# Performance work log

Hardware: AMD Instinct MI355X
Metric: run time of the kernel (lower is better)

The kernel has to match this reference:

```python
import jax, jax.numpy as jnp
import numpy as np

N = 32768; D = 384; P = 3; CORR_D = 2 * 49 * P * P  # 882
G_KK = 4096; G_JK = 512
EPS = 1e-3  # LayerNorm eps in the torch module

FLOAT_NAMES = ("net","inp","corr","corr_w1","corr_b1","corr_w2","corr_b2","corr_ln_g","corr_ln_b","corr_w3","corr_b3","norm_g","norm_b","c1_w1","c1_b1","c1_w2","c1_b2","c2_w1","c2_b1","c2_w2","c2_b2","kk_fw","kk_fb","kk_gw","kk_gb","kk_hw","kk_hb","ij_fw","ij_fb","ij_gw","ij_gb","ij_hw","ij_hb","g_ln1_g","g_ln1_b","g1_gw","g1_gb","g1_r1w","g1_r1b","g1_r2w","g1_r2b","g_ln2_g","g_ln2_b","g2_gw","g2_gb","g2_r1w","g2_r1b","g2_r2w","g2_r2b","d_w","d_b","w_w","w_b")

def _ln(x, g, b):
    m = jnp.mean(x, -1, keepdims=True)
    v = jnp.mean((x - m) ** 2, -1, keepdims=True)
    return (x - m) * jax.lax.rsqrt(v + EPS) * g + b

def _mlp2(x, w1, b1, w2, b2):
    return jax.nn.relu(x @ w1 + b1) @ w2 + b2

def _gated_residual(x, gw, gb, r1w, r1b, r2w, r2b):
    gate = jax.nn.sigmoid(x @ gw + gb)
    res = jax.nn.relu(x @ r1w + r1b) @ r2w + r2b
    return x + gate * res

def _soft_agg(x, jx, fw, fb, gw, gb, hw, hb, num_groups):
    # x: [N, D]; jx: [N] group ids -> group-wise softmax weighted sum
    logits = x @ gw + gb
    feats = x @ fw + fb
    gmax = jax.ops.segment_max(logits, jx, num_segments=num_groups)
    e = jnp.exp(logits - gmax[jx])
    den = jax.ops.segment_sum(e, jx, num_segments=num_groups)
    w = e / (den[jx] + 1e-12)
    y = jax.ops.segment_sum(feats * w, jx, num_segments=num_groups)
    return (y @ hw + hb)[jx]

def _forward(p, nix, njx, ukk, ujk):
    # corr encoder MLP
    h = jax.nn.relu(p["corr"] @ p["corr_w1"] + p["corr_b1"]) @ p["corr_w2"] + p["corr_b2"]
    h = jax.nn.relu(_ln(h, p["corr_ln_g"], p["corr_ln_b"])) @ p["corr_w3"] + p["corr_b3"]
    net = p["net"] + p["inp"] + h
    net = _ln(net, p["norm_g"], p["norm_b"])
    mask_ix = (nix >= 0).astype(net.dtype).reshape(1, -1, 1)
    mask_jx = (njx >= 0).astype(net.dtype).reshape(1, -1, 1)
    net = net + _mlp2(mask_ix * net[:, nix], p["c1_w1"], p["c1_b1"], p["c1_w2"], p["c1_b2"])
    net = net + _mlp2(mask_jx * net[:, njx], p["c2_w1"], p["c2_b1"], p["c2_w2"], p["c2_b2"])
    net = net + _soft_agg(net[0], ukk, p["kk_fw"], p["kk_fb"], p["kk_gw"], p["kk_gb"], p["kk_hw"], p["kk_hb"], G_KK)[None]
    net = net + _soft_agg(net[0], ujk, p["ij_fw"], p["ij_fb"], p["ij_gw"], p["ij_gb"], p["ij_hw"], p["ij_hb"], G_JK)[None]
    net = _ln(net, p["g_ln1_g"], p["g_ln1_b"])
    net = _gated_residual(net, p["g1_gw"], p["g1_gb"], p["g1_r1w"], p["g1_r1b"], p["g1_r2w"], p["g1_r2b"])
    net = _ln(net, p["g_ln2_g"], p["g_ln2_b"])
    net = _gated_residual(net, p["g2_gw"], p["g2_gb"], p["g2_r1w"], p["g2_r1b"], p["g2_r2w"], p["g2_r2b"])
    r = jax.nn.relu(net)
    d = r @ p["d_w"] + p["d_b"]               # GradClip is identity in forward
    w = jax.nn.sigmoid(r @ p["w_w"] + p["w_b"])
    return net, d, w

def setup_inputs() -> dict:
    key = jax.random.key(0)
    it = iter(jax.random.split(key, 64))
    def pr(*shape):
        return jax.random.normal(next(it), shape, dtype=jnp.float32) * 0.02
    z = lambda *s: jnp.zeros(s, jnp.float32)
    o = lambda *s: jnp.ones(s, jnp.float32)
    inp = {
        "net": jax.random.normal(next(it), (1, N, D), dtype=jnp.float32),
        "inp": jax.random.normal(next(it), (1, N, D), dtype=jnp.float32),
        "corr": jax.random.normal(next(it), (1, N, CORR_D), dtype=jnp.float32),
        "nix": jax.random.randint(next(it), (N,), 0, N),
        "njx": jax.random.randint(next(it), (N,), 0, N),
        "ukk": jax.random.randint(next(it), (N,), 0, G_KK),
        "ujk": jax.random.randint(next(it), (N,), 0, G_JK),
        "corr_w1": pr(CORR_D, D), "corr_b1": z(D), "corr_w2": pr(D, D), "corr_b2": z(D),
        "corr_ln_g": o(D), "corr_ln_b": z(D), "corr_w3": pr(D, D), "corr_b3": z(D),
        "norm_g": o(D), "norm_b": z(D),
        "c1_w1": pr(D, D), "c1_b1": z(D), "c1_w2": pr(D, D), "c1_b2": z(D),
        "c2_w1": pr(D, D), "c2_b1": z(D), "c2_w2": pr(D, D), "c2_b2": z(D),
        "kk_fw": pr(D, D), "kk_fb": z(D), "kk_gw": pr(D, D), "kk_gb": z(D), "kk_hw": pr(D, D), "kk_hb": z(D),
        "ij_fw": pr(D, D), "ij_fb": z(D), "ij_gw": pr(D, D), "ij_gb": z(D), "ij_hw": pr(D, D), "ij_hb": z(D),
        "g_ln1_g": o(D), "g_ln1_b": z(D),
        "g1_gw": pr(D, D), "g1_gb": z(D), "g1_r1w": pr(D, D), "g1_r1b": z(D), "g1_r2w": pr(D, D), "g1_r2b": z(D),
        "g_ln2_g": o(D), "g_ln2_b": z(D),
        "g2_gw": pr(D, D), "g2_gb": z(D), "g2_r1w": pr(D, D), "g2_r1b": z(D), "g2_r2w": pr(D, D), "g2_r2b": z(D),
        "d_w": pr(D, 2), "d_b": z(2), "w_w": pr(D, 2), "w_b": z(2),
    }
    return inp

def reference(net, inp, corr, corr_w1, corr_b1, corr_w2, corr_b2, corr_ln_g, corr_ln_b, corr_w3, corr_b3, norm_g, norm_b, c1_w1, c1_b1, c1_w2, c1_b2, c2_w1, c2_b1, c2_w2, c2_b2, kk_fw, kk_fb, kk_gw, kk_gb, kk_hw, kk_hb, ij_fw, ij_fb, ij_gw, ij_gb, ij_hw, ij_hb, g_ln1_g, g_ln1_b, g1_gw, g1_gb, g1_r1w, g1_r1b, g1_r2w, g1_r2b, g_ln2_g, g_ln2_b, g2_gw, g2_gb, g2_r1w, g2_r1b, g2_r2w, g2_r2b, d_w, d_b, w_w, w_b, nix, njx, ukk, ujk):
    loc = locals()
    fl = {k: loc[k] for k in FLOAT_NAMES}
    return _forward(fl, nix, njx, ukk, ujk)
```

## Files before the change

kernel.cpp:

```cpp
#include <hip/hip_runtime.h>
#include <hip/hip_bf16.h>
#include <math.h>

#define NR 32768
#define DD 384
#define CDM 882
#define CDMP 896

typedef float f4 __attribute__((ext_vector_type(4)));
typedef float f32x4 __attribute__((ext_vector_type(4)));
typedef __bf16 bf16x8 __attribute__((ext_vector_type(8)));
typedef __bf16 bf16x4 __attribute__((ext_vector_type(4)));

__device__ inline f4 ld4(const float* p) { f4 v; __builtin_memcpy(&v, p, 16); return v; }
__device__ inline void st4(float* p, f4 v) { __builtin_memcpy(p, &v, 16); }
__device__ inline bf16x8 ld8h(const __bf16* p) { bf16x8 v; __builtin_memcpy(&v, p, 16); return v; }
__device__ inline void st8h(__bf16* p, bf16x8 v) { __builtin_memcpy(p, &v, 16); }

__device__ inline void gl_lds16(const void* g, void* l) {
  __builtin_amdgcn_global_load_lds(
      (const __attribute__((address_space(1))) void*)g,
      (__attribute__((address_space(3))) void*)l, 16, 0, 0);
}

__device__ inline float gred16(float v) {
#pragma unroll
  for (int o = 1; o < 16; o <<= 1) v += __shfl_xor(v, o, 64);
  return v;
}

__global__ __launch_bounds__(256) void corr2bf16_k(const float* __restrict__ src,
                                                   __bf16* __restrict__ dst) {
  int i = blockIdx.x * 256 + threadIdx.x;
  int row = i / 112, c8 = (i - row * 112) * 8;
  const float* sp = src + (size_t)row * CDM + c8;
  bf16x8 h;
  if (c8 + 8 <= CDM) {
#pragma unroll
    for (int e = 0; e < 8; ++e) h[e] = (__bf16)sp[e];
  } else {
#pragma unroll
    for (int e = 0; e < 8; ++e) h[e] = (c8 + e < CDM) ? (__bf16)sp[e] : (__bf16)0.f;
  }
  st8h(dst + (size_t)row * CDMP + c8, h);
}

struct WPtrs { const float* w[18]; };

__global__ __launch_bounds__(256) void trans_all_k(WPtrs P, __bf16* __restrict__ dst) {
  int wi = blockIdx.y;
  const float* W = P.w[wi];
  __bf16* WT = dst + (size_t)wi * DD * DD;
  int i = blockIdx.x * 256 + threadIdx.x;
  if (i >= DD * DD) return;
  int n = i / DD, k = i - n * DD;
  WT[i] = (__bf16)W[(size_t)k * DD + n];
}

__global__ __launch_bounds__(256) void trans_corr_k(const float* __restrict__ W,
                                                    __bf16* __restrict__ WT) {
  int i = blockIdx.x * 256 + threadIdx.x;
  if (i >= DD * CDMP) return;
  int n = i / CDMP, k = i - n * CDMP;
  WT[i] = (k < CDM) ? (__bf16)W[(size_t)k * DD + n] : (__bf16)0.f;
}

struct GP {
  const void* A; const __bf16* WT; const float* bias; __bf16* OUT;
  const __bf16* XRES; const __bf16* GIN;
  const float* p0; const float* p1; const float* p2; const float* p3;
  float* fout; const float* net32; const float* inp32;
  const int* idx; const __bf16* zpage; int M; int K;
};

template <int EPI, int AFP32>
__global__ __launch_bounds__(512, 1) void gemm_k(GP gp) {
  __shared__ __align__(16) __bf16 sm[2 * 32768];
  const int t = threadIdx.x;
  const int w = t >> 6, lane = t & 63;
  const int m0 = blockIdx.x * 128;
  const int fr = lane & 15, fq = lane >> 4;
  const int wr = (w >> 2) * 64, wc = (w & 3) * 96;
  const int K = gp.K;

  const __bf16* aptr[2];
  int aadv[2];
  const __bf16* bptr[6];
#pragma unroll
  for (int j = 0; j < 2; ++j) {
    int rloc = w * 16 + j * 8 + (lane >> 3);
    int cch = (lane & 7) ^ (rloc & 7);
    if constexpr (!AFP32) {
      int ar = gp.idx ? gp.idx[m0 + rloc] : (m0 + rloc);
      if (ar >= 0) { aptr[j] = (const __bf16*)gp.A + (size_t)ar * K + cch * 8; aadv[j] = 64; }
      else { aptr[j] = gp.zpage; aadv[j] = 0; }
    }
  }
#pragma unroll
  for (int j = 0; j < 6; ++j) {
    int rloc = w * 48 + j * 8 + (lane >> 3);
    int cch = (lane & 7) ^ (rloc & 7);
    bptr[j] = gp.WT + (size_t)rloc * K + cch * 8;
  }
  const float* Af = (const float*)gp.A;
  const int NT = K >> 6;

  f32x4 acc[4][6];
#pragma unroll
  for (int a = 0; a < 4; ++a)
#pragma unroll
    for (int b = 0; b < 6; ++b)
#pragma unroll
      for (int j = 0; j < 4; ++j) acc[a][b][j] = 0.f;

  auto stageG = [&](int buf) {
    __bf16* As = sm + buf * 32768;
    __bf16* Bs = As + 8192;
#pragma unroll
    for (int j = 0; j < 2; ++j) {
      gl_lds16(aptr[j], &As[(w * 16 + j * 8) * 64]);
      aptr[j] += aadv[j];
    }
#pragma unroll
    for (int j = 0; j < 6; ++j) {
      gl_lds16(bptr[j], &Bs[(w * 48 + j * 8) * 64]);
      bptr[j] += 64;
    }
  };

  auto stageF = [&](int k0) {
    __bf16* As = sm;
    __bf16* Bs = sm + 8192;
#pragma unroll
    for (int j = 0; j < 2; ++j) {
      int rr = (t >> 3) + 64 * j;
      int cc = t & 7;
      const float* ap = Af + (size_t)(m0 + rr) * K + k0 + cc * 8;
      f4 v0 = ld4(ap), v1 = ld4(ap + 4);
      bf16x8 h;
#pragma unroll
      for (int e = 0; e < 4; ++e) { h[e] = (__bf16)v0[e]; h[4 + e] = (__bf16)v1[e]; }
      *reinterpret_cast<bf16x8*>(&As[rr * 64 + ((cc ^ (rr & 7)) << 3)]) = h;
    }
#pragma unroll
    for (int j = 0; j < 6; ++j) {
      gl_lds16(bptr[j], &Bs[(w * 48 + j * 8) * 64]);
      bptr[j] += 64;
    }
  };

  auto compute = [&](int buf) {
    const __bf16* As = sm + buf * 32768;
    const __bf16* Bs = As + 8192;
#pragma unroll
    for (int kk2 = 0; kk2 < 2; ++kk2) {
      bf16x8 af[4];
      bf16x8 bv[6];
#pragma unroll
      for (int mi = 0; mi < 4; ++mi) {
        int rr = wr + mi * 16 + fr;
        af[mi] = *reinterpret_cast<const bf16x8*>(
            &As[rr * 64 + (((fq + kk2 * 4) ^ (rr & 7)) << 3)]);
      }
#pragma unroll
      for (int ni = 0; ni < 6; ++ni) {
        int rr = wc + ni * 16 + fr;
        bv[ni] = *reinterpret_cast<const bf16x8*>(
            &Bs[rr * 64 + (((fq + kk2 * 4) ^ (rr & 7)) << 3)]);
      }
#pragma unroll
      for (int mi = 0; mi < 4; ++mi)
#pragma unroll
        for (int ni = 0; ni < 6; ++ni)
          acc[mi][ni] = __builtin_amdgcn_mfma_f32_16x16x32_bf16(af[mi], bv[ni],
                                                                acc[mi][ni], 0, 0, 0);
    }
  };

  if constexpr (AFP32) {
    for (int tt = 0; tt < NT; ++tt) {
      if (tt) __syncthreads();
      stageF(tt << 6);
      __syncthreads();
      compute(0);
    }
  } else {
    stageG(0);
    int buf = 0;
    for (int tt = 0; tt < NT; ++tt) {
      if (tt + 1 < NT) {
        stageG(buf ^ 1);
        asm volatile("s_waitcnt vmcnt(8)" ::: "memory");
      } else {
        asm volatile("s_waitcnt vmcnt(0)" ::: "memory");
      }
      __builtin_amdgcn_s_barrier();
      __builtin_amdgcn_sched_barrier(0);
      compute(buf);
      __builtin_amdgcn_s_barrier();
      __builtin_amdgcn_sched_barrier(0);
      buf ^= 1;
    }
  }

  const int nw = w & 3;
  float bcol[6];
#pragma unroll
  for (int ni = 0; ni < 6; ++ni) bcol[ni] = gp.bias[wc + ni * 16 + fr];
#pragma unroll
  for (int mi = 0; mi < 4; ++mi)
#pragma unroll
    for (int ni = 0; ni < 6; ++ni)
#pragma unroll
      for (int j = 0; j < 4; ++j) acc[mi][ni][j] += bcol[ni];

  if constexpr (EPI <= 2) {
#pragma unroll
    for (int mi = 0; mi < 4; ++mi)
#pragma unroll
      for (int ni = 0; ni < 6; ++ni) {
        int col = wc + ni * 16 + fr;
#pragma unroll
        for (int j = 0; j < 4; ++j) {
          int row = m0 + wr + mi * 16 + fq * 4 + j;
          size_t o = (size_t)row * DD + col;
          float v = acc[mi][ni][j];
          if constexpr (EPI == 0) gp.OUT[o] = (__bf16)v;
          else if constexpr (EPI == 1) gp.OUT[o] = (__bf16)fmaxf(v, 0.f);
          else gp.OUT[o] = (__bf16)((float)gp.OUT[o] + v);
        }
      }
  } else {
    if constexpr (EPI == 5) {
#pragma unroll
      for (int mi = 0; mi < 4; ++mi)
#pragma unroll
        for (int ni = 0; ni < 6; ++ni) {
          int col = wc + ni * 16 + fr;
#pragma unroll
          for (int j = 0; j < 4; ++j) {
            int row = m0 + wr + mi * 16 + fq * 4 + j;
            size_t o = (size_t)row * DD + col;
            acc[mi][ni][j] += gp.net32[o] + gp.inp32[o];
          }
        }
    }
    if constexpr (EPI == 6 || EPI == 7) {
#pragma unroll
      for (int mi = 0; mi < 4; ++mi)
#pragma unroll
        for (int ni = 0; ni < 6; ++ni) {
          int col = wc + ni * 16 + fr;
#pragma unroll
          for (int j = 0; j < 4; ++j) {
            int row = m0 + wr + mi * 16 + fq * 4 + j;
            size_t o = (size_t)row * DD + col;
            float gl = (float)gp.GIN[o];
            float sg = 1.f / (1.f + expf(-gl));
            acc[mi][ni][j] = (float)gp.XRES[o] + sg * acc[mi][ni][j];
          }
        }
    }
    __syncthreads();
    if constexpr (EPI != 7) {
      float s1[4][4], s2[4][4];
#pragma unroll
      for (int mi = 0; mi < 4; ++mi)
#pragma unroll
        for (int j = 0; j < 4; ++j) { s1[mi][j] = 0.f; s2[mi][j] = 0.f; }
#pragma unroll
      for (int mi = 0; mi < 4; ++mi)
#pragma unroll
        for (int ni = 0; ni < 6; ++ni)
#pragma unroll
          for (int j = 0; j < 4; ++j) {
            float v = acc[mi][ni][j];
            s1[mi][j] += v;
            s2[mi][j] += v * v;
          }
#pragma unroll
      for (int o = 1; o < 16; o <<= 1)
#pragma unroll
        for (int mi = 0; mi < 4; ++mi)
#pragma unroll
          for (int j = 0; j < 4; ++j) {
            s1[mi][j] += __shfl_xor(s1[mi][j], o, 64);
            s2[mi][j] += __shfl_xor(s2[mi][j], o, 64);
          }
      float* lsum = (float*)sm;
      float* lsq = lsum + 512;
      if (fr == 0) {
#pragma unroll
        for (int mi = 0; mi < 4; ++mi)
#pragma unroll
          for (int j = 0; j < 4; ++j) {
            int rr = wr + mi * 16 + fq * 4 + j;
            lsum[rr * 4 + nw] = s1[mi][j];
            lsq[rr * 4 + nw] = s2[mi][j];
          }
      }
      __syncthreads();
      float mn[4][4], rs[4][4];
#pragma unroll
      for (int mi = 0; mi < 4; ++mi)
#pragma unroll
        for (int j = 0; j < 4; ++j) {
          int rr = wr + mi * 16 + fq * 4 + j;
          float S1 = lsum[rr * 4] + lsum[rr * 4 + 1] + lsum[rr * 4 + 2] + lsum[rr * 4 + 3];
          float S2 = lsq[rr * 4] + lsq[rr * 4 + 1] + lsq[rr * 4 + 2] + lsq[rr * 4 + 3];
          float m = S1 * (1.f / 384.f);
          float va = S2 * (1.f / 384.f) - m * m;
          mn[mi][j] = m;
          rs[mi][j] = rsqrtf(va + 1e-3f);
        }
#pragma unroll
      for (int ni = 0; ni < 6; ++ni) {
        int col = wc + ni * 16 + fr;
        float gg = gp.p0[col], bb = gp.p1[col];
#pragma unroll
        for (int mi = 0; mi < 4; ++mi)
#pragma unroll
          for (int j = 0; j < 4; ++j) {
            int row = m0 + wr + mi * 16 + fq * 4 + j;
            float y = (acc[mi][ni][j] - mn[mi][j]) * rs[mi][j] * gg + bb;
            if constexpr (EPI == 4) y = fmaxf(y, 0.f);
            gp.OUT[(size_t)row * DD + col] = (__bf16)y;
          }
      }
    } else {
      float c0[6], c1[6], c2[6], c3[6];
#pragma unroll
      for (int ni = 0; ni < 6; ++ni) {
        int col = wc + ni * 16 + fr;
        c0[ni] = gp.p0[2 * col];
        c1[ni] = gp.p0[2 * col + 1];
        c2[ni] = gp.p2[2 * col];
        c3[ni] = gp.p2[2 * col + 1];
      }
      float dt[4][4][4];
#pragma unroll
      for (int mi = 0; mi < 4; ++mi)
#pragma unroll
        for (int j = 0; j < 4; ++j)
#pragma unroll
          for (int q = 0; q < 4; ++q) dt[mi][j][q] = 0.f;
#pragma unroll
      for (int mi = 0; mi < 4; ++mi)
#pragma unroll
        for (int ni = 0; ni < 6; ++ni) {
          int col = wc + ni * 16 + fr;
#pragma unroll
          for (int j = 0; j < 4; ++j) {
            int row = m0 + wr + mi * 16 + fq * 4 + j;
            float v = acc[mi][ni][j];
            gp.fout[(size_t)row * DD + col] = v;
            float r = fmaxf(v, 0.f);
            dt[mi][j][0] += r * c0[ni];
            dt[mi][j][1] += r * c1[ni];
            dt[mi][j][2] += r * c2[ni];
            dt[mi][j][3] += r * c3[ni];
          }
        }
#pragma unroll
      for (int o = 1; o < 16; o <<= 1)
#pragma unroll
        for (int mi = 0; mi < 4; ++mi)
#pragma unroll
          for (int j = 0; j < 4; ++j)
#pragma unroll
            for (int q = 0; q < 4; ++q)
              dt[mi][j][q] += __shfl_xor(dt[mi][j][q], o, 64);
      float* lt = (float*)sm;
      if (fr == 0) {
#pragma unroll
        for (int mi = 0; mi < 4; ++mi)
#pragma unroll
          for (int j = 0; j < 4; ++j) {
            int rr = wr + mi * 16 + fq * 4 + j;
#pragma unroll
            for (int q = 0; q < 4; ++q) lt[(rr * 4 + nw) * 4 + q] = dt[mi][j][q];
          }
      }
      __syncthreads();
      if (nw == 0 && fr == 0) {
        float* fd = gp.fout + (size_t)NR * DD;
        float* fw = fd + (size_t)NR * 2;
#pragma unroll
        for (int mi = 0; mi < 4; ++mi)
#pragma unroll
          for (int j = 0; j < 4; ++j) {
            int rr = wr + mi * 16 + fq * 4 + j;
            int row = m0 + rr;
            float T[4];
#pragma unroll
            for (int q = 0; q < 4; ++q)
              T[q] = lt[(rr * 4 + 0) * 4 + q] + lt[(rr * 4 + 1) * 4 + q] +
                     lt[(rr * 4 + 2) * 4 + q] + lt[(rr * 4 + 3) * 4 + q];
            fd[2 * row] = T[0] + gp.p1[0];
            fd[2 * row + 1] = T[1] + gp.p1[1];
            fw[2 * row] = 1.f / (1.f + expf(-(T[2] + gp.p3[0])));
            fw[2 * row + 1] = 1.f / (1.f + expf(-(T[3] + gp.p3[1])));
          }
      }
    }
  }
}

__global__ __launch_bounds__(256) void ln_ag_k(const __bf16* __restrict__ X,
                                               const __bf16* __restrict__ z,
                                               const int* __restrict__ gid,
                                               const float* __restrict__ g,
                                               const float* __restrict__ b,
                                               __bf16* __restrict__ out) {
  int w = threadIdx.x >> 6, lane = threadIdx.x & 63;
  int s = lane & 15, qq = lane >> 4;
  int row = blockIdx.x * 16 + w * 4 + qq;
  int gr = gid[row];
  size_t base = (size_t)row * DD;
  size_t zbase = (size_t)gr * DD;
  float v[24];
#pragma unroll
  for (int i = 0; i < 3; ++i) {
    int col = (s + 16 * i) * 8;
    bf16x8 h = ld8h(X + base + col);
    bf16x8 zz = ld8h(z + zbase + col);
#pragma unroll
    for (int e = 0; e < 8; ++e) v[i * 8 + e] = (float)h[e] + (float)zz[e];
  }
  float sm = 0.f;
#pragma unroll
  for (int i = 0; i < 24; ++i) sm += v[i];
  sm = gred16(sm);
  float mean = sm * (1.f / 384.f);
  float qs = 0.f;
#pragma unroll
  for (int i = 0; i < 24; ++i) { float d = v[i] - mean; qs += d * d; }
  qs = gred16(qs);
  float rs = rsqrtf(qs * (1.f / 384.f) + 1e-3f);
#pragma unroll
  for (int i = 0; i < 3; ++i) {
    int col = (s + 16 * i) * 8;
    f4 g0 = ld4(g + col), g1 = ld4(g + col + 4);
    f4 b0 = ld4(b + col), b1 = ld4(b + col + 4);
    bf16x8 o;
#pragma unroll
    for (int e = 0; e < 4; ++e) {
      o[e] = (__bf16)((v[i * 8 + e] - mean) * rs * g0[e] + b0[e]);
      o[4 + e] = (__bf16)((v[i * 8 + 4 + e] - mean) * rs * g1[e] + b1[e]);
    }
    st8h(out + base + col, o);
  }
}

__global__ __launch_bounds__(256) void hist2_k(const int* __restrict__ ukk,
                                               const int* __restrict__ ujk,
                                               int* __restrict__ ckk,
                                               int* __restrict__ cij) {
  int i = blockIdx.x * 256 + threadIdx.x;
  atomicAdd(&ckk[ukk[i]], 1);
  atomicAdd(&cij[ujk[i]], 1);
}

__device__ inline void scan_body(const int* cnt, int* off, int* curb, int G, int* ls) {
  int t = threadIdx.x;
  int per = G / 256;
  int base = t * per;
  int s = 0;
  for (int i = 0; i < per; ++i) s += cnt[base + i];
  ls[t] = s;
  __syncthreads();
  for (int o = 1; o < 256; o <<= 1) {
    int v = (t >= o) ? ls[t - o] : 0;
    __syncthreads();
    ls[t] += v;
    __syncthreads();
  }
  int run = (t == 0) ? 0 : ls[t - 1];
  for (int i = 0; i < per; ++i) {
    off[base + i] = run;
    run += cnt[base + i];
    curb[base + i] = 0;
  }
  if (t == 255) off[G] = run;
}

__global__ __launch_bounds__(256) void scan2_k(const int* ckk, int* okk, int* qkk,
                                               const int* cij, int* oij, int* qij) {
  __shared__ int ls[256];
  if (blockIdx.x == 0) scan_body(ckk, okk, qkk, 4096, ls);
  else scan_body(cij, oij, qij, 512, ls);
}

__global__ __launch_bounds__(256) void scatter2_k(const int* __restrict__ ukk,
                                                  const int* __restrict__ ujk,
                                                  const int* __restrict__ okk,
                                                  int* __restrict__ qkk,
                                                  int* __restrict__ rkk,
                                                  const int* __restrict__ oij,
                                                  int* __restrict__ qij,
                                                  int* __restrict__ rij) {
  int i = blockIdx.x * 256 + threadIdx.x;
  int g1 = ukk[i];
  rkk[okk[g1] + atomicAdd(&qkk[g1], 1)] = i;
  int g2 = ujk[i];
  rij[oij[g2] + atomicAdd(&qij[g2], 1)] = i;
}

__global__ __launch_bounds__(384) void segagg_k(const __bf16* __restrict__ L,
                                                const __bf16* __restrict__ Ft,
                                                const int* __restrict__ rows,
                                                const int* __restrict__ off,
                                                float* __restrict__ yb) {
  int g = blockIdx.x;
  int c = threadIdx.x;
  int s = off[g], e = off[g + 1];
  float mx = -3.0e38f;
  for (int p = s; p < e; ++p) {
    int r = rows[p];
    mx = fmaxf(mx, (float)L[(size_t)r * DD + c]);
  }
  float num = 0.f, den = 0.f;
  for (int p = s; p < e; ++p) {
    int r = rows[p];
    float lv = (float)L[(size_t)r * DD + c];
    float fv = (float)Ft[(size_t)r * DD + c];
    float ev = expf(lv - mx);
    den += ev;
    num += fv * ev;
  }
  yb[(size_t)g * DD + c] = num / (den + 1e-12f);
}

__global__ __launch_bounds__(256) void addgather_k(__bf16* __restrict__ X,
                                                   const __bf16* __restrict__ z,
                                                   const int* __restrict__ gid) {
  int i = blockIdx.x * 256 + threadIdx.x;
  int row = i / 48, c = (i - row * 48) * 8;
  int g = gid[row];
  size_t lo = (size_t)row * DD + c;
  bf16x8 a = ld8h(X + lo);
  bf16x8 zz = ld8h(z + (size_t)g * DD + c);
  bf16x8 o;
#pragma unroll
  for (int e = 0; e < 8; ++e) o[e] = (__bf16)((float)a[e] + (float)zz[e]);
  st8h(X + lo, o);
}

extern "C" void kernel_launch(void* const* d_in, const int* in_sizes, int n_in,
                              void* d_out, int out_size, void* d_ws, size_t ws_size,
                              hipStream_t stream) {
  const float* in_net = (const float*)d_in[0];
  const float* in_inp = (const float*)d_in[1];
  const float* in_corr = (const float*)d_in[2];
  const int* nix = (const int*)d_in[3];
  const int* njx = (const int*)d_in[4];
  const int* ukk = (const int*)d_in[5];
  const int* ujk = (const int*)d_in[6];
  auto F = [&](int i) { return (const float*)d_in[i]; };

  constexpr size_t MiB = 1024 * 1024;
  constexpr size_t SZ_ACT = (size_t)NR * DD * 2;
  char* ws = (char*)d_ws;
  __bf16* Xc = (__bf16*)(ws);
  __bf16* T2b = (__bf16*)(ws);
  __bf16* Fb = (__bf16*)(ws + SZ_ACT);
  __bf16* zb = (__bf16*)(ws + 2 * SZ_ACT);
  float* yb = (float*)(ws + 2 * SZ_ACT + 3 * MiB);
  __bf16* T1b = (__bf16*)(ws + 60 * MiB);
  char* p = ws + 84 * MiB;
  int* rows_kk = (int*)p; p += (size_t)NR * 4;
  int* rows_ij = (int*)p; p += (size_t)NR * 4;
  int* off_kk = (int*)p; p += 8192 * 4;
  int* off_ij = (int*)p; p += 1024 * 4;
  int* cnt_kk = (int*)p; p += 4096 * 4;
  int* cnt_ij = (int*)p; p += 512 * 4;
  int* curb_kk = (int*)p; p += 4096 * 4;
  int* curb_ij = (int*)p; p += 512 * 4;
  __bf16* wt_all = (__bf16*)p; p += (size_t)18 * DD * DD * 2;
  __bf16* wt_corr1 = (__bf16*)p; p += (size_t)DD * CDMP * 2;
  __bf16* zpage = (__bf16*)p;

  const int widx[18] = {17, 19, 21, 23, 25, 27, 29, 31, 33, 35, 39, 41, 43, 47, 49, 51, 9, 13};
  WPtrs P;
  for (int i = 0; i < 18; ++i) P.w[i] = F(widx[i]);
  auto WTp = [&](int i) { return wt_all + (size_t)i * DD * DD; };

  hipMemsetAsync(zpage, 0, 256, stream);
  hipMemsetAsync(cnt_kk, 0, 4096 * 4, stream);
  hipMemsetAsync(cnt_ij, 0, 512 * 4, stream);
  trans_all_k<<<dim3(576, 18), 256, 0, stream>>>(P, wt_all);
  trans_corr_k<<<1344, 256, 0, stream>>>(F(7), wt_corr1);
  corr2bf16_k<<<NR * 112 / 256, 256, 0, stream>>>(in_corr, Xc);
  hist2_k<<<NR / 256, 256, 0, stream>>>(ukk, ujk, cnt_kk, cnt_ij);
  scan2_k<<<2, 256, 0, stream>>>(cnt_kk, off_kk, curb_kk, cnt_ij, off_ij, curb_ij);
  scatter2_k<<<NR / 256, 256, 0, stream>>>(ukk, ujk, off_kk, curb_kk, rows_kk,
                                           off_ij, curb_ij, rows_ij);

  auto G = [&](int epi, const void* A, const __bf16* WT, const float* bias,
               __bf16* OUT, const __bf16* XRES, const __bf16* GIN,
               const float* p0, const float* p1, const float* p2, const float* p3,
               float* fout, const float* n32, const float* i32,
               const int* idx, int M, int K) {
    GP gp{A, WT, bias, OUT, XRES, GIN, p0, p1, p2, p3, fout, n32, i32, idx, zpage, M, K};
    dim3 g(M / 128), b(512);
    switch (epi) {
      case 0: gemm_k<0, 0><<<g, b, 0, stream>>>(gp); break;
      case 1: gemm_k<1, 0><<<g, b, 0, stream>>>(gp); break;
      case 2: gemm_k<2, 0><<<g, b, 0, stream>>>(gp); break;
      case 4: gemm_k<4, 0><<<g, b, 0, stream>>>(gp); break;
      case 5: gemm_k<5, 0><<<g, b, 0, stream>>>(gp); break;
      case 6: gemm_k<6, 0><<<g, b, 0, stream>>>(gp); break;
      case 7: gemm_k<7, 0><<<g, b, 0, stream>>>(gp); break;
      case 8: gemm_k<0, 1><<<g, b, 0, stream>>>(gp); break;
    }
  };
  auto GS = [&](int epi, const void* A, const __bf16* WT, const float* bias,
                __bf16* OUT, const int* idx, int M, int K) {
    G(epi, A, WT, bias, OUT, nullptr, nullptr, nullptr, nullptr, nullptr, nullptr,
      nullptr, nullptr, nullptr, idx, M, K);
  };

  const int SEGB = NR * 48 / 256;

  GS(1, Xc, wt_corr1, F(8), T1b, nullptr, NR, CDMP);
  G(4, T1b, WTp(16), F(10), T2b, nullptr, nullptr, F(11), F(12), nullptr, nullptr,
    nullptr, nullptr, nullptr, nullptr, NR, DD);
  G(5, T2b, WTp(17), F(14), T1b, nullptr, nullptr, F(15), F(16), nullptr, nullptr,
    nullptr, in_net, in_inp, nullptr, NR, DD);
  GS(1, T1b, WTp(0), F(18), T2b, nix, NR, DD);
  GS(2, T2b, WTp(1), F(20), T1b, nullptr, NR, DD);
  GS(1, T1b, WTp(2), F(22), T2b, njx, NR, DD);
  GS(2, T2b, WTp(3), F(24), T1b, nullptr, NR, DD);
  GS(0, T1b, WTp(5), F(28), T2b, nullptr, NR, DD);
  GS(0, T1b, WTp(4), F(26), Fb, nullptr, NR, DD);
  segagg_k<<<4096, 384, 0, stream>>>(T2b, Fb, rows_kk, off_kk, yb);
  GS(8, yb, WTp(6), F(30), zb, nullptr, 4096, DD);
  addgather_k<<<SEGB, 256, 0, stream>>>(T1b, zb, ukk);
  GS(0, T1b, WTp(8), F(34), T2b, nullptr, NR, DD);
  GS(0, T1b, WTp(7), F(32), Fb, nullptr, NR, DD);
  segagg_k<<<512, 384, 0, stream>>>(T2b, Fb, rows_ij, off_ij, yb);
  GS(8, yb, WTp(9), F(36), zb, nullptr, 512, DD);
  ln_ag_k<<<NR / 16, 256, 0, stream>>>(T1b, zb, ujk, F(37), F(38), T2b);
  GS(0, T2b, WTp(10), F(40), Fb, nullptr, NR, DD);
  GS(1, T2b, WTp(11), F(42), T1b, nullptr, NR, DD);
  G(6, T1b, WTp(12), F(44), T2b, T2b, Fb, F(45), F(46), nullptr, nullptr,
    nullptr, nullptr, nullptr, nullptr, NR, DD);
  GS(0, T2b, WTp(13), F(48), Fb, nullptr, NR, DD);
  GS(1, T2b, WTp(14), F(50), T1b, nullptr, NR, DD);
  G(7, T1b, WTp(15), F(52), nullptr, T2b, Fb, F(53), F(54), F(55), F(56),
    (float*)d_out, nullptr, nullptr, nullptr, NR, DD);
}
```

Baseline: 608.0 us.

## Shrink GEMM row tile to 64, single-buffer LDS, two blocks per CU, XCD swizzle

The GEMM kernel now uses a 64-row tile instead of 128, halving accumulators and using a smaller single-buffered LDS tile, with launch bounds set for two blocks per CU. Block indices are remapped so consecutive row tiles land on the same XCD for L2 locality. The residual epilogue now reads a separate XRES buffer instead of updating in place, and the buffer assignments are adjusted to match. This doubles the grid and raises occupancy at the cost of losing the explicit double-buffered load/compute overlap and re-reading weights more often.

```diff
diff --git a/kernel.cpp b/kernel.cpp
--- a/kernel.cpp
+++ b/kernel.cpp
@@ -10,7 +10,6 @@
 typedef float f4 __attribute__((ext_vector_type(4)));
 typedef float f32x4 __attribute__((ext_vector_type(4)));
 typedef __bf16 bf16x8 __attribute__((ext_vector_type(8)));
-typedef __bf16 bf16x4 __attribute__((ext_vector_type(4)));
 
 __device__ inline f4 ld4(const float* p) { f4 v; __builtin_memcpy(&v, p, 16); return v; }
 __device__ inline void st4(float* p, f4 v) { __builtin_memcpy(p, &v, 16); }
@@ -27,6 +26,11 @@
 #pragma unroll
   for (int o = 1; o < 16; o <<= 1) v += __shfl_xor(v, o, 64);
   return v;
+}
+
+__device__ inline int xcd_swz(int orig, int nwg) {
+  int q = nwg >> 3, r = nwg & 7, xcd = orig & 7, lid = orig >> 3;
+  return (xcd < r ? xcd * (q + 1) : r * (q + 1) + (xcd - r) * q) + lid;
 }
 
 __global__ __launch_bounds__(256) void corr2bf16_k(const float* __restrict__ src,
@@ -73,142 +77,17 @@
   const int* idx; const __bf16* zpage; int M; int K;
 };
 
-template <int EPI, int AFP32>
-__global__ __launch_bounds__(512, 1) void gemm_k(GP gp) {
-  __shared__ __align__(16) __bf16 sm[2 * 32768];
-  const int t = threadIdx.x;
-  const int w = t >> 6, lane = t & 63;
-  const int m0 = blockIdx.x * 128;
+template <int EPI>
+__device__ __forceinline__ void epilogue(const GP& gp, f32x4 (&acc)[2][6],
+                                         __bf16* sm, int m0, int w, int lane) {
   const int fr = lane & 15, fq = lane >> 4;
-  const int wr = (w >> 2) * 64, wc = (w & 3) * 96;
-  const int K = gp.K;
-
-  const __bf16* aptr[2];
-  int aadv[2];
-  const __bf16* bptr[6];
-#pragma unroll
-  for (int j = 0; j < 2; ++j) {
-    int rloc = w * 16 + j * 8 + (lane >> 3);
-    int cch = (lane & 7) ^ (rloc & 7);
-    if constexpr (!AFP32) {
-      int ar = gp.idx ? gp.idx[m0 + rloc] : (m0 + rloc);
-      if (ar >= 0) { aptr[j] = (const __bf16*)gp.A + (size_t)ar * K + cch * 8; aadv[j] = 64; }
-      else { aptr[j] = gp.zpage; aadv[j] = 0; }
-    }
-  }
-#pragma unroll
-  for (int j = 0; j < 6; ++j) {
-    int rloc = w * 48 + j * 8 + (lane >> 3);
-    int cch = (lane & 7) ^ (rloc & 7);
-    bptr[j] = gp.WT + (size_t)rloc * K + cch * 8;
-  }
-  const float* Af = (const float*)gp.A;
-  const int NT = K >> 6;
-
-  f32x4 acc[4][6];
-#pragma unroll
-  for (int a = 0; a < 4; ++a)
-#pragma unroll
-    for (int b = 0; b < 6; ++b)
-#pragma unroll
-      for (int j = 0; j < 4; ++j) acc[a][b][j] = 0.f;
-
-  auto stageG = [&](int buf) {
-    __bf16* As = sm + buf * 32768;
-    __bf16* Bs = As + 8192;
-#pragma unroll
-    for (int j = 0; j < 2; ++j) {
-      gl_lds16(aptr[j], &As[(w * 16 + j * 8) * 64]);
-      aptr[j] += aadv[j];
-    }
-#pragma unroll
-    for (int j = 0; j < 6; ++j) {
-      gl_lds16(bptr[j], &Bs[(w * 48 + j * 8) * 64]);
-      bptr[j] += 64;
-    }
-  };
-
-  auto stageF = [&](int k0) {
-    __bf16* As = sm;
-    __bf16* Bs = sm + 8192;
-#pragma unroll
-    for (int j = 0; j < 2; ++j) {
-      int rr = (t >> 3) + 64 * j;
-      int cc = t & 7;
-      const float* ap = Af + (size_t)(m0 + rr) * K + k0 + cc * 8;
-      f4 v0 = ld4(ap), v1 = ld4(ap + 4);
-      bf16x8 h;
-#pragma unroll
-      for (int e = 0; e < 4; ++e) { h[e] = (__bf16)v0[e]; h[4 + e] = (__bf16)v1[e]; }
-      *reinterpret_cast<bf16x8*>(&As[rr * 64 + ((cc ^ (rr & 7)) << 3)]) = h;
-    }
-#pragma unroll
-    for (int j = 0; j < 6; ++j) {
-      gl_lds16(bptr[j], &Bs[(w * 48 + j * 8) * 64]);
-      bptr[j] += 64;
-    }
-  };
-
-  auto compute = [&](int buf) {
-    const __bf16* As = sm + buf * 32768;
-    const __bf16* Bs = As + 8192;
-#pragma unroll
-    for (int kk2 = 0; kk2 < 2; ++kk2) {
-      bf16x8 af[4];
-      bf16x8 bv[6];
-#pragma unroll
-      for (int mi = 0; mi < 4; ++mi) {
-        int rr = wr + mi * 16 + fr;
-        af[mi] = *reinterpret_cast<const bf16x8*>(
-            &As[rr * 64 + (((fq + kk2 * 4) ^ (rr & 7)) << 3)]);
-      }
-#pragma unroll
-      for (int ni = 0; ni < 6; ++ni) {
-        int rr = wc + ni * 16 + fr;
-        bv[ni] = *reinterpret_cast<const bf16x8*>(
-            &Bs[rr * 64 + (((fq + kk2 * 4) ^ (rr & 7)) << 3)]);
-      }
-#pragma unroll
-      for (int mi = 0; mi < 4; ++mi)
-#pragma unroll
-        for (int ni = 0; ni < 6; ++ni)
-          acc[mi][ni] = __builtin_amdgcn_mfma_f32_16x16x32_bf16(af[mi], bv[ni],
-                                                                acc[mi][ni], 0, 0, 0);
-    }
-  };
-
-  if constexpr (AFP32) {
-    for (int tt = 0; tt < NT; ++tt) {
-      if (tt) __syncthreads();
-      stageF(tt << 6);
-      __syncthreads();
-      compute(0);
-    }
-  } else {
-    stageG(0);
-    int buf = 0;
-    for (int tt = 0; tt < NT; ++tt) {
-      if (tt + 1 < NT) {
-        stageG(buf ^ 1);
-        asm volatile("s_waitcnt vmcnt(8)" ::: "memory");
-      } else {
-        asm volatile("s_waitcnt vmcnt(0)" ::: "memory");
-      }
-      __builtin_amdgcn_s_barrier();
-      __builtin_amdgcn_sched_barrier(0);
-      compute(buf);
-      __builtin_amdgcn_s_barrier();
-      __builtin_amdgcn_sched_barrier(0);
-      buf ^= 1;
-    }
-  }
-
+  const int wr = (w >> 2) * 32, wc = (w & 3) * 96;
   const int nw = w & 3;
   float bcol[6];
 #pragma unroll
   for (int ni = 0; ni < 6; ++ni) bcol[ni] = gp.bias[wc + ni * 16 + fr];
 #pragma unroll
-  for (int mi = 0; mi < 4; ++mi)
+  for (int mi = 0; mi < 2; ++mi)
 #pragma unroll
     for (int ni = 0; ni < 6; ++ni)
 #pragma unroll
@@ -216,7 +95,7 @@
 
   if constexpr (EPI <= 2) {
 #pragma unroll
-    for (int mi = 0; mi < 4; ++mi)
+    for (int mi = 0; mi < 2; ++mi)
 #pragma unroll
       for (int ni = 0; ni < 6; ++ni) {
         int col = wc + ni * 16 + fr;
@@ -227,13 +106,13 @@
           float v = acc[mi][ni][j];
           if constexpr (EPI == 0) gp.OUT[o] = (__bf16)v;
           else if constexpr (EPI == 1) gp.OUT[o] = (__bf16)fmaxf(v, 0.f);
-          else gp.OUT[o] = (__bf16)((float)gp.OUT[o] + v);
+          else gp.OUT[o] = (__bf16)((float)gp.XRES[o] + v);
         }
       }
   } else {
     if constexpr (EPI == 5) {
 #pragma unroll
-      for (int mi = 0; mi < 4; ++mi)
+      for (int mi = 0; mi < 2; ++mi)
 #pragma unroll
         for (int ni = 0; ni < 6; ++ni) {
           int col = wc + ni * 16 + fr;
@@ -247,7 +126,7 @@
     }
     if constexpr (EPI == 6 || EPI == 7) {
 #pragma unroll
-      for (int mi = 0; mi < 4; ++mi)
+      for (int mi = 0; mi < 2; ++mi)
 #pragma unroll
         for (int ni = 0; ni < 6; ++ni) {
           int col = wc + ni * 16 + fr;
@@ -263,13 +142,13 @@
     }
     __syncthreads();
     if constexpr (EPI != 7) {
-      float s1[4][4], s2[4][4];
-#pragma unroll
-      for (int mi = 0; mi < 4; ++mi)
+      float s1[2][4], s2[2][4];
+#pragma unroll
+      for (int mi = 0; mi < 2; ++mi)
 #pragma unroll
         for (int j = 0; j < 4; ++j) { s1[mi][j] = 0.f; s2[mi][j] = 0.f; }
 #pragma unroll
-      for (int mi = 0; mi < 4; ++mi)
+      for (int mi = 0; mi < 2; ++mi)
 #pragma unroll
         for (int ni = 0; ni < 6; ++ni)
 #pragma unroll
@@ -281,17 +160,17 @@
 #pragma unroll
       for (int o = 1; o < 16; o <<= 1)
 #pragma unroll
-        for (int mi = 0; mi < 4; ++mi)
+        for (int mi = 0; mi < 2; ++mi)
 #pragma unroll
           for (int j = 0; j < 4; ++j) {
             s1[mi][j] += __shfl_xor(s1[mi][j], o, 64);
             s2[mi][j] += __shfl_xor(s2[mi][j], o, 64);
           }
       float* lsum = (float*)sm;
-      float* lsq = lsum + 512;
+      float* lsq = lsum + 256;
       if (fr == 0) {
 #pragma unroll
-        for (int mi = 0; mi < 4; ++mi)
+        for (int mi = 0; mi < 2; ++mi)
 #pragma unroll
           for (int j = 0; j < 4; ++j) {
             int rr = wr + mi * 16 + fq * 4 + j;
@@ -300,9 +179,9 @@
           }
       }
       __syncthreads();
-      float mn[4][4], rs[4][4];
-#pragma unroll
-      for (int mi = 0; mi < 4; ++mi)
+      float mn[2][4], rs[2][4];
+#pragma unroll
+      for (int mi = 0; mi < 2; ++mi)
 #pragma unroll
         for (int j = 0; j < 4; ++j) {
           int rr = wr + mi * 16 + fq * 4 + j;
@@ -318,7 +197,7 @@
         int col = wc + ni * 16 + fr;
         float gg = gp.p0[col], bb = gp.p1[col];
 #pragma unroll
-        for (int mi = 0; mi < 4; ++mi)
+        for (int mi = 0; mi < 2; ++mi)
 #pragma unroll
           for (int j = 0; j < 4; ++j) {
             int row = m0 + wr + mi * 16 + fq * 4 + j;
@@ -337,15 +216,15 @@
         c2[ni] = gp.p2[2 * col];
         c3[ni] = gp.p2[2 * col + 1];
       }
-      float dt[4][4][4];
-#pragma unroll
-      for (int mi = 0; mi < 4; ++mi)
+      float dt[2][4][4];
+#pragma unroll
+      for (int mi = 0; mi < 2; ++mi)
 #pragma unroll
         for (int j = 0; j < 4; ++j)
 #pragma unroll
           for (int q = 0; q < 4; ++q) dt[mi][j][q] = 0.f;
 #pragma unroll
-      for (int mi = 0; mi < 4; ++mi)
+      for (int mi = 0; mi < 2; ++mi)
 #pragma unroll
         for (int ni = 0; ni < 6; ++ni) {
           int col = wc + ni * 16 + fr;
@@ -364,7 +243,7 @@
 #pragma unroll
       for (int o = 1; o < 16; o <<= 1)
 #pragma unroll
-        for (int mi = 0; mi < 4; ++mi)
+        for (int mi = 0; mi < 2; ++mi)
 #pragma unroll
           for (int j = 0; j < 4; ++j)
 #pragma unroll
@@ -373,7 +252,7 @@
       float* lt = (float*)sm;
       if (fr == 0) {
 #pragma unroll
-        for (int mi = 0; mi < 4; ++mi)
+        for (int mi = 0; mi < 2; ++mi)
 #pragma unroll
           for (int j = 0; j < 4; ++j) {
             int rr = wr + mi * 16 + fq * 4 + j;
@@ -386,7 +265,7 @@
         float* fd = gp.fout + (size_t)NR * DD;
         float* fw = fd + (size_t)NR * 2;
 #pragma unroll
-        for (int mi = 0; mi < 4; ++mi)
+        for (int mi = 0; mi < 2; ++mi)
 #pragma unroll
           for (int j = 0; j < 4; ++j) {
             int rr = wr + mi * 16 + fq * 4 + j;
@@ -404,6 +283,99 @@
       }
     }
   }
+}
+
+__device__ __forceinline__ void mfma_block64(const __bf16* As, const __bf16* Bs,
+                                             f32x4 (&acc)[2][6], int wr, int wc,
+                                             int fr, int fq) {
+#pragma unroll
+  for (int kk2 = 0; kk2 < 2; ++kk2) {
+    bf16x8 af[2];
+    bf16x8 bv[6];
+#pragma unroll
+    for (int mi = 0; mi < 2; ++mi) {
+      int rr = wr + mi * 16 + fr;
+      af[mi] = *reinterpret_cast<const bf16x8*>(
+          &As[rr * 64 + (((fq + kk2 * 4) ^ (rr & 7)) << 3)]);
+    }
+#pragma unroll
+    for (int ni = 0; ni < 6; ++ni) {
+      int rr = wc + ni * 16 + fr;
+      bv[ni] = *reinterpret_cast<const bf16x8*>(
+          &Bs[rr * 64 + (((fq + kk2 * 4) ^ (rr & 7)) << 3)]);
+    }
+#pragma unroll
+    for (int mi = 0; mi < 2; ++mi)
+#pragma unroll
+      for (int ni = 0; ni < 6; ++ni)
+        acc[mi][ni] = __builtin_amdgcn_mfma_f32_16x16x32_bf16(af[mi], bv[ni],
+                                                              acc[mi][ni], 0, 0, 0);
+  }
+}
+
+template <int EPI, int AFP32>
+__global__ __launch_bounds__(512, 2) void gemm_k(GP gp) {
+  __shared__ __align__(16) __bf16 sm[28672];
+  const int t = threadIdx.x;
+  const int w = t >> 6, lane = t & 63;
+  const int m0 = xcd_swz(blockIdx.x, gridDim.x) * 64;
+  const int fr = lane & 15, fq = lane >> 4;
+  const int wr = (w >> 2) * 32, wc = (w & 3) * 96;
+  const int K = gp.K;
+  __bf16* As = sm;
+  __bf16* Bs = sm + 4096;
+
+  const __bf16* bptr[6];
+#pragma unroll
+  for (int j = 0; j < 6; ++j) {
+    int rloc = w * 48 + j * 8 + (lane >> 3);
+    int cch = (lane & 7) ^ (rloc & 7);
+    bptr[j] = gp.WT + (size_t)rloc * K + cch * 8;
+  }
+  const __bf16* aptr = nullptr;
+  int aadv = 0;
+  if constexpr (!AFP32) {
+    int arow = w * 8 + (lane >> 3);
+    int acch = (lane & 7) ^ (arow & 7);
+    int ar = gp.idx ? gp.idx[m0 + arow] : (m0 + arow);
+    if (ar >= 0) { aptr = (const __bf16*)gp.A + (size_t)ar * K + acch * 8; aadv = 64; }
+    else { aptr = gp.zpage; aadv = 0; }
+  }
+  const float* Af = (const float*)gp.A;
+  const int NT = K >> 6;
+
+  f32x4 acc[2][6];
+#pragma unroll
+  for (int a = 0; a < 2; ++a)
+#pragma unroll
+    for (int b = 0; b < 6; ++b)
+#pragma unroll
+      for (int j = 0; j < 4; ++j) acc[a][b][j] = 0.f;
+
+  for (int tt = 0; tt < NT; ++tt) {
+    if (tt) __syncthreads();
+    if constexpr (AFP32) {
+      int rr = t >> 3, cc = t & 7;
+      const float* ap = Af + (size_t)(m0 + rr) * K + (tt << 6) + cc * 8;
+      f4 v0 = ld4(ap), v1 = ld4(ap + 4);
+      bf16x8 h;
+#pragma unroll
+      for (int e = 0; e < 4; ++e) { h[e] = (__bf16)v0[e]; h[4 + e] = (__bf16)v1[e]; }
+      *reinterpret_cast<bf16x8*>(&As[rr * 64 + ((cc ^ (rr & 7)) << 3)]) = h;
+    } else {
+      gl_lds16(aptr, &As[(w * 8) * 64]);
+      aptr += aadv;
+    }
+#pragma unroll
+    for (int j = 0; j < 6; ++j) {
+      gl_lds16(bptr[j], &Bs[(w * 48 + j * 8) * 64]);
+      bptr[j] += 64;
+    }
+    __syncthreads();
+    mfma_block64(As, Bs, acc, wr, wc, fr, fq);
+  }
+  __syncthreads();
+  epilogue<EPI>(gp, acc, sm, m0, w, lane);
 }
 
 __global__ __launch_bounds__(256) void ln_ag_k(const __bf16* __restrict__ X,
@@ -596,13 +568,20 @@
   scatter2_k<<<NR / 256, 256, 0, stream>>>(ukk, ujk, off_kk, curb_kk, rows_kk,
                                            off_ij, curb_ij, rows_ij);
 
-  auto G = [&](int epi, const void* A, const __bf16* WT, const float* bias,
-               __bf16* OUT, const __bf16* XRES, const __bf16* GIN,
-               const float* p0, const float* p1, const float* p2, const float* p3,
-               float* fout, const float* n32, const float* i32,
-               const int* idx, int M, int K) {
-    GP gp{A, WT, bias, OUT, XRES, GIN, p0, p1, p2, p3, fout, n32, i32, idx, zpage, M, K};
-    dim3 g(M / 128), b(512);
+  auto mkGP = [&]() {
+    GP g{};
+    g.zpage = zpage;
+    g.K = DD;
+    g.M = NR;
+    return g;
+  };
+
+  auto launch = [&](int epi, int afp32, const GP& gp) {
+    dim3 g(gp.M / 64), b(512);
+    if (afp32) {
+      gemm_k<0, 1><<<g, b, 0, stream>>>(gp);
+      return;
+    }
     switch (epi) {
       case 0: gemm_k<0, 0><<<g, b, 0, stream>>>(gp); break;
       case 1: gemm_k<1, 0><<<g, b, 0, stream>>>(gp); break;
@@ -611,42 +590,86 @@
       case 5: gemm_k<5, 0><<<g, b, 0, stream>>>(gp); break;
       case 6: gemm_k<6, 0><<<g, b, 0, stream>>>(gp); break;
       case 7: gemm_k<7, 0><<<g, b, 0, stream>>>(gp); break;
-      case 8: gemm_k<0, 1><<<g, b, 0, stream>>>(gp); break;
     }
   };
-  auto GS = [&](int epi, const void* A, const __bf16* WT, const float* bias,
-                __bf16* OUT, const int* idx, int M, int K) {
-    G(epi, A, WT, bias, OUT, nullptr, nullptr, nullptr, nullptr, nullptr, nullptr,
-      nullptr, nullptr, nullptr, idx, M, K);
-  };
 
   const int SEGB = NR * 48 / 256;
 
-  GS(1, Xc, wt_corr1, F(8), T1b, nullptr, NR, CDMP);
-  G(4, T1b, WTp(16), F(10), T2b, nullptr, nullptr, F(11), F(12), nullptr, nullptr,
-    nullptr, nullptr, nullptr, nullptr, NR, DD);
-  G(5, T2b, WTp(17), F(14), T1b, nullptr, nullptr, F(15), F(16), nullptr, nullptr,
-    nullptr, in_net, in_inp, nullptr, NR, DD);
-  GS(1, T1b, WTp(0), F(18), T2b, nix, NR, DD);
-  GS(2, T2b, WTp(1), F(20), T1b, nullptr, NR, DD);
-  GS(1, T1b, WTp(2), F(22), T2b, njx, NR, DD);
-  GS(2, T2b, WTp(3), F(24), T1b, nullptr, NR, DD);
-  GS(0, T1b, WTp(5), F(28), T2b, nullptr, NR, DD);
-  GS(0, T1b, WTp(4), F(26), Fb, nullptr, NR, DD);
+  {
+    GP g = mkGP(); g.A = Xc; g.WT = wt_corr1; g.bias = F(8); g.OUT = T1b; g.K = CDMP;
+    launch(1, 0, g);
+  }
+  {
+    GP g = mkGP(); g.A = T1b; g.WT = WTp(16); g.bias = F(10); g.OUT = T2b;
+    g.p0 = F(11); g.p1 = F(12);
+    launch(4, 0, g);
+  }
+  {
+    GP g = mkGP(); g.A = T2b; g.WT = WTp(17); g.bias = F(14); g.OUT = T1b;
+    g.p0 = F(15); g.p1 = F(16); g.net32 = in_net; g.inp32 = in_inp;
+    launch(5, 0, g);
+  }
+  {
+    GP g = mkGP(); g.A = T1b; g.WT = WTp(0); g.bias = F(18); g.OUT = T2b; g.idx = nix;
+    launch(1, 0, g);
+  }
+  {
+    GP g = mkGP(); g.A = T2b; g.WT = WTp(1); g.bias = F(20); g.OUT = Fb; g.XRES = T1b;
+    launch(2, 0, g);
+  }
+  {
+    GP g = mkGP(); g.A = Fb; g.WT = WTp(2); g.bias = F(22); g.OUT = T2b; g.idx = njx;
+    launch(1, 0, g);
+  }
+  {
+    GP g = mkGP(); g.A = T2b; g.WT = WTp(3); g.bias = F(24); g.OUT = T1b; g.XRES = Fb;
+    launch(2, 0, g);
+  }
+  {
+    GP g = mkGP(); g.A = T1b; g.WT = WTp(5); g.bias = F(28); g.OUT = T2b;
+    launch(0, 0, g);
+    g.WT = WTp(4); g.bias = F(26); g.OUT = Fb;
+    launch(0, 0, g);
+  }
   segagg_k<<<4096, 384, 0, stream>>>(T2b, Fb, rows_kk, off_kk, yb);
-  GS(8, yb, WTp(6), F(30), zb, nullptr, 4096, DD);
+  {
+    GP g = mkGP(); g.A = yb; g.WT = WTp(6); g.bias = F(30); g.OUT = zb; g.M = 4096;
+    launch(0, 1, g);
+  }
   addgather_k<<<SEGB, 256, 0, stream>>>(T1b, zb, ukk);
-  GS(0, T1b, WTp(8), F(34), T2b, nullptr, NR, DD);
-  GS(0, T1b, WTp(7), F(32), Fb, nullptr, NR, DD);
+  {
+    GP g = mkGP(); g.A = T1b; g.WT = WTp(8); g.bias = F(34); g.OUT = T2b;
+    launch(0, 0, g);
+    g.WT = WTp(7); g.bias = F(32); g.OUT = Fb;
+    launch(0, 0, g);
+  }
   segagg_k<<<512, 384, 0, stream>>>(T2b, Fb, rows_ij, off_ij, yb);
-  GS(8, yb, WTp(9), F(36), zb, nullptr, 512, DD);
+  {
+    GP g = mkGP(); g.A = yb; g.WT = WTp(9); g.bias = F(36); g.OUT = zb; g.M = 512;
+    launch(0, 1, g);
+  }
   ln_ag_k<<<NR / 16, 256, 0, stream>>>(T1b, zb, ujk, F(37), F(38), T2b);
-  GS(0, T2b, WTp(10), F(40), Fb, nullptr, NR, DD);
-  GS(1, T2b, WTp(11), F(42), T1b, nullptr, NR, DD);
-  G(6, T1b, WTp(12), F(44), T2b, T2b, Fb, F(45), F(46), nullptr, nullptr,
-    nullptr, nullptr, nullptr, nullptr, NR, DD);
-  GS(0, T2b, WTp(13), F(48), Fb, nullptr, NR, DD);
-  GS(1, T2b, WTp(14), F(50), T1b, nullptr, NR, DD);
-  G(7, T1b, WTp(15), F(52), nullptr, T2b, Fb, F(53), F(54), F(55), F(56),
-    (float*)d_out, nullptr, nullptr, nullptr, NR, DD);
-}
+  {
+    GP g = mkGP(); g.A = T2b; g.WT = WTp(10); g.bias = F(40); g.OUT = Fb;
+    launch(0, 0, g);
+    g.WT = WTp(11); g.bias = F(42); g.OUT = T1b;
+    launch(1, 0, g);
+  }
+  {
+    GP g = mkGP(); g.A = T1b; g.WT = WTp(12); g.bias = F(44); g.OUT = T2b;
+    g.XRES = T2b; g.GIN = Fb; g.p0 = F(45); g.p1 = F(46);
+    launch(6, 0, g);
+  }
+  {
+    GP g = mkGP(); g.A = T2b; g.WT = WTp(13); g.bias = F(48); g.OUT = Fb;
+    launch(0, 0, g);
+    g.WT = WTp(14); g.bias = F(50); g.OUT = T1b;
+    launch(1, 0, g);
+  }
+  {
+    GP g = mkGP(); g.A = T1b; g.WT = WTp(15); g.bias = F(52);
+    g.XRES = T2b; g.GIN = Fb; g.p0 = F(53); g.p1 = F(54); g.p2 = F(55); g.p3 = F(56);
+    g.fout = (float*)d_out;
+    launch(7, 0, g);
+  }
+}
```

New measurement: 642.8 us. +5.7%, slower.
